# Kernel optimization log

Hardware: AMD Instinct MI355X
Metric: run time of the kernel (lower is better)

The kernel has to match this reference:

```python
import jax, jax.numpy as jnp
import numpy as np

B, N, F, U = 4, 4096, 256, 128
NEG = -1.0e9


def setup_inputs() -> dict:
    key = jax.random.key(0)
    k1, k2, k3, k4, k5 = jax.random.split(key, 5)
    inputs = jax.random.normal(k1, (B, N, F), dtype=jnp.float32)
    # Glorot-normal-like scales
    w = jax.random.normal(k2, (F, U), dtype=jnp.float32) * np.sqrt(2.0 / (F + U)).astype(np.float32)
    ai = jax.random.normal(k3, (U, N), dtype=jnp.float32) * np.sqrt(2.0 / (U + N)).astype(np.float32)
    aj = jax.random.normal(k4, (U, N), dtype=jnp.float32) * np.sqrt(2.0 / (U + N)).astype(np.float32)
    a = (jax.random.uniform(k5, (N, N)) < 0.004).astype(jnp.float32)
    adj = jnp.maximum(a, a.T)
    return {"inputs": inputs, "w": w, "ai": ai, "aj": aj, "adj": adj}


def reference(inputs, w, ai, aj, adj):
    # f: [B, N, U]
    f = jnp.einsum('bnf,fu->bnu', inputs, w)
    # self_attn[b,i,j] = (f ai)[b,i,j]; other_attn = transpose([0,2,1]) of (f aj)
    self_attn = jnp.einsum('bnu,um->bnm', f, ai)          # [B, N, N]
    other_attn = jnp.einsum('bnu,um->bmn', f, aj)         # transposed [B, N, N]
    mask = adj + jnp.eye(N, dtype=adj.dtype)              # allow self + neighbors
    attn = self_attn + other_attn + NEG * (1.0 - mask)
    attn = jax.nn.softmax(attn, axis=1)                   # softmax over rows (axis=1)
    # out[b,j,u] = sum_i f[b,i,u] * attn[b,i,j]
    out = jnp.einsum('biu,bij->bju', f, attn)
    return jax.nn.relu(out), attn
```

## Files before the change

kernel.cpp:

```cpp
#include <hip/hip_runtime.h>
#include <hip/hip_bf16.h>

#define NN 4096
#define UU 128
#define BB 4
#define FF 256
#define MAXD 128

__global__ __launch_bounds__(256) void transpose2(const float* __restrict__ ai,
                                                  const float* __restrict__ aj,
                                                  float* __restrict__ aiT,
                                                  float* __restrict__ ajT) {
    __shared__ float tile[32][33];
    const float* src = blockIdx.z ? aj : ai;
    float* dst = blockIdx.z ? ajT : aiT;
    int n0 = blockIdx.x * 32;
    int u0 = blockIdx.y * 32;
    int tx = threadIdx.x;
    int ty = threadIdx.y;
    for (int r = 0; r < 32; r += 8)
        tile[ty + r][tx] = src[(size_t)(u0 + ty + r) * NN + n0 + tx];
    __syncthreads();
    for (int r = 0; r < 32; r += 8)
        dst[(size_t)(n0 + ty + r) * UU + u0 + tx] = tile[tx][ty + r];
}

__global__ __launch_bounds__(256) void fgemm(const float* __restrict__ A,
                                             const float* __restrict__ Wm,
                                             float* __restrict__ F) {
    __shared__ float As[64][68];
    __shared__ float Ws[64][132];
    int t = threadIdx.x;
    int r0 = blockIdx.x * 64;
    int cg = t & 31;
    int rg = t >> 5;
    float acc[8][4] = {};

    for (int kc = 0; kc < FF; kc += 64) {
        {
            int row = t >> 2;
            int kb = (t & 3) * 16;
#pragma unroll
            for (int q = 0; q < 4; q++) {
                int kq = kb + q * 4;
                float4 v = *(const float4*)(A + (size_t)(r0 + row) * FF + kc + kq);
                As[kq + 0][row] = v.x; As[kq + 1][row] = v.y;
                As[kq + 2][row] = v.z; As[kq + 3][row] = v.w;
            }
        }
        {
#pragma unroll
            for (int q = 0; q < 8; q++) {
                int idx = q * 256 + t;
                int k = idx >> 5;
                int c4 = (idx & 31) * 4;
                *(float4*)&Ws[k][c4] = *(const float4*)(Wm + (size_t)(kc + k) * UU + c4);
            }
        }
        __syncthreads();
#pragma unroll 4
        for (int kk = 0; kk < 64; kk++) {
            float4 a0 = *(const float4*)&As[kk][rg * 8];
            float4 a1 = *(const float4*)&As[kk][rg * 8 + 4];
            float4 w4 = *(const float4*)&Ws[kk][cg * 4];
            float av[8] = {a0.x, a0.y, a0.z, a0.w, a1.x, a1.y, a1.z, a1.w};
#pragma unroll
            for (int i = 0; i < 8; i++) {
                acc[i][0] += av[i] * w4.x;
                acc[i][1] += av[i] * w4.y;
                acc[i][2] += av[i] * w4.z;
                acc[i][3] += av[i] * w4.w;
            }
        }
        __syncthreads();
    }
#pragma unroll
    for (int i = 0; i < 8; i++) {
        *(float4*)(F + (size_t)(r0 + rg * 8 + i) * UU + cg * 4) =
            make_float4(acc[i][0], acc[i][1], acc[i][2], acc[i][3]);
    }
}

__global__ __launch_bounds__(256) void scan_adj(const float* __restrict__ adj,
                                                unsigned short* __restrict__ csc,
                                                int* __restrict__ cnt,
                                                int* __restrict__ dblf) {
    __shared__ unsigned short tmp[MAXD];
    __shared__ int c, d;
    int j = blockIdx.x, tid = threadIdx.x;
    if (tid == 0) { c = 0; d = 0; }
    __syncthreads();
    const float4* row = (const float4*)(adj + (size_t)j * NN);
#pragma unroll
    for (int k = 0; k < 4; k++) {
        int q = tid + k * 256;
        float4 v = row[q];
        int base = q * 4;
        float vals[4] = {v.x, v.y, v.z, v.w};
#pragma unroll
        for (int t = 0; t < 4; t++) {
            int i = base + t;
            bool nz = (vals[t] != 0.0f);
            if (i == j) { if (nz) d = 1; nz = true; }
            if (nz) {
                int p = atomicAdd(&c, 1);
                if (p < MAXD) tmp[p] = (unsigned short)i;
            }
        }
    }
    __syncthreads();
    int M = c < MAXD ? c : MAXD;
    if (tid < M) csc[(size_t)j * MAXD + tid] = tmp[tid];
    if (tid == 0) { cnt[j] = M; dblf[j] = d; }
}

__global__ __launch_bounds__(256) void gat_cols(const unsigned short* __restrict__ csc,
                                                const int* __restrict__ cnt,
                                                const int* __restrict__ dblf,
                                                const float* __restrict__ f,
                                                const float* __restrict__ aiT,
                                                const float* __restrict__ ajT,
                                                float* __restrict__ out,
                                                float* __restrict__ attn) {
    __shared__ unsigned short sidx[MAXD];
    __shared__ float sex[BB][MAXD];
    int j = blockIdx.x, tid = threadIdx.x;
    int lane = tid & 63, b = tid >> 6;
    int M = cnt[j];
    int oneh = dblf[j];
    if (tid < M) sidx[tid] = csc[(size_t)j * MAXD + tid];

    const float* fb = f + (size_t)b * NN * UU;
    float2 fj = *(const float2*)(fb + (size_t)j * UU + 2 * lane);

    if (oneh) {
        if (lane == 0) attn[((size_t)(b * NN + j)) * NN + j] = 1.0f;
        float2 o;
        o.x = fj.x > 0.0f ? fj.x : 0.0f;
        o.y = fj.y > 0.0f ? fj.y : 0.0f;
        *(float2*)(out + ((size_t)(b * NN + j)) * UU + 2 * lane) = o;
        return;
    }
    __syncthreads();

    float2 ai2 = *(const float2*)(aiT + (size_t)j * UU + 2 * lane);
    float denom = 0.0f, acc0 = 0.0f, acc1 = 0.0f;
    for (int e = 0; e < M; e++) {
        int i = sidx[e];
        float2 fi  = *(const float2*)(fb + (size_t)i * UU + 2 * lane);
        float2 aj2 = *(const float2*)(ajT + (size_t)i * UU + 2 * lane);
        float p = fi.x * ai2.x + fi.y * ai2.y + fj.x * aj2.x + fj.y * aj2.y;
#pragma unroll
        for (int off = 32; off > 0; off >>= 1) p += __shfl_xor(p, off);
        float ex = __expf(p);
        denom += ex;
        acc0 += ex * fi.x;
        acc1 += ex * fi.y;
        if (lane == 0) sex[b][e] = ex;
    }
    float inv = 1.0f / denom;

    float2 o;
    o.x = acc0 * inv; o.y = acc1 * inv;
    o.x = o.x > 0.0f ? o.x : 0.0f;
    o.y = o.y > 0.0f ? o.y : 0.0f;
    *(float2*)(out + ((size_t)(b * NN + j)) * UU + 2 * lane) = o;

    __syncthreads();
    for (int e = lane; e < M; e += 64)
        attn[((size_t)(b * NN + sidx[e])) * NN + j] = sex[b][e] * inv;
}

extern "C" void kernel_launch(void* const* d_in, const int* in_sizes, int n_in,
                              void* d_out, int out_size, void* d_ws, size_t ws_size,
                              hipStream_t stream) {
    const float* inputs = (const float*)d_in[0];
    const float* w      = (const float*)d_in[1];
    const float* ai     = (const float*)d_in[2];
    const float* aj     = (const float*)d_in[3];
    const float* adj    = (const float*)d_in[4];

    float* out  = (float*)d_out;
    float* attn = out + (size_t)BB * NN * UU;

    float* f   = (float*)d_ws;
    float* aiT = f + (size_t)BB * NN * UU;
    float* ajT = aiT + (size_t)NN * UU;
    unsigned short* csc = (unsigned short*)(ajT + (size_t)NN * UU);
    int* cnt  = (int*)(csc + (size_t)NN * MAXD);
    int* dblf = cnt + NN;

    hipMemsetAsync(attn, 0, (size_t)BB * NN * NN * sizeof(float), stream);

    transpose2<<<dim3(NN / 32, UU / 32, 2), dim3(32, 8), 0, stream>>>(ai, aj, aiT, ajT);
    fgemm<<<dim3((BB * NN) / 64), 256, 0, stream>>>(inputs, w, f);
    scan_adj<<<NN, 256, 0, stream>>>(adj, csc, cnt, dblf);
    gat_cols<<<NN, 256, 0, stream>>>(csc, cnt, dblf, f, aiT, ajT, out, attn);
}
```

Before: 449.7 us.

## Batch neighbor loads and replace per-edge shuffle reductions with LDS chunked sums

The gat_cols edge loop is split into two passes. The first pass issues 16 neighbor feature loads per chunk, writes the partial dot products to LDS, and lets one lane per edge sum them and apply exp. The second pass accumulates the exp-weighted features in unrolled groups of 8. This removes the serial per-edge chain of load, wavefront shuffle reduction and exp, and exposes more memory-level parallelism. In exchange it reads the neighbor features twice (the second read likely hits cache), uses more LDS, and relies on wavefront-lockstep ordering of LDS writes and reads within each batch's wave, with no explicit barrier.

```diff
diff --git a/kernel.cpp b/kernel.cpp
--- a/kernel.cpp
+++ b/kernel.cpp
@@ -6,6 +6,7 @@
 #define BB 4
 #define FF 256
 #define MAXD 128
+#define CH 16
 
 __global__ __launch_bounds__(256) void transpose2(const float* __restrict__ ai,
                                                   const float* __restrict__ aj,
@@ -123,12 +124,13 @@
                                                 float* __restrict__ out,
                                                 float* __restrict__ attn) {
     __shared__ unsigned short sidx[MAXD];
-    __shared__ float sex[BB][MAXD];
+    __shared__ float sexp[BB][MAXD];
+    __shared__ float part[BB][CH][68];
     int j = blockIdx.x, tid = threadIdx.x;
     int lane = tid & 63, b = tid >> 6;
     int M = cnt[j];
     int oneh = dblf[j];
-    if (tid < M) sidx[tid] = csc[(size_t)j * MAXD + tid];
+    if (tid < MAXD) sidx[tid] = csc[(size_t)j * MAXD + tid];
 
     const float* fb = f + (size_t)b * NN * UU;
     float2 fj = *(const float2*)(fb + (size_t)j * UU + 2 * lane);
@@ -144,21 +146,45 @@
     __syncthreads();
 
     float2 ai2 = *(const float2*)(aiT + (size_t)j * UU + 2 * lane);
-    float denom = 0.0f, acc0 = 0.0f, acc1 = 0.0f;
-    for (int e = 0; e < M; e++) {
-        int i = sidx[e];
-        float2 fi  = *(const float2*)(fb + (size_t)i * UU + 2 * lane);
-        float2 aj2 = *(const float2*)(ajT + (size_t)i * UU + 2 * lane);
-        float p = fi.x * ai2.x + fi.y * ai2.y + fj.x * aj2.x + fj.y * aj2.y;
-#pragma unroll
-        for (int off = 32; off > 0; off >>= 1) p += __shfl_xor(p, off);
-        float ex = __expf(p);
-        denom += ex;
-        acc0 += ex * fi.x;
-        acc1 += ex * fi.y;
-        if (lane == 0) sex[b][e] = ex;
-    }
+    float denom = 0.0f;
+
+    for (int e0 = 0; e0 < M; e0 += CH) {
+#pragma unroll
+        for (int cc = 0; cc < CH; cc++) {
+            int ee = e0 + cc;
+            int i = sidx[ee < M ? ee : M - 1];
+            float2 fi  = *(const float2*)(fb + (size_t)i * UU + 2 * lane);
+            float2 aj2 = *(const float2*)(ajT + (size_t)i * UU + 2 * lane);
+            part[b][cc][lane] = fi.x * ai2.x + fi.y * ai2.y + fj.x * aj2.x + fj.y * aj2.y;
+        }
+        if (lane < CH && e0 + lane < M) {
+            float s = 0.0f;
+#pragma unroll
+            for (int q = 0; q < 16; q++) {
+                float4 v = *(const float4*)&part[b][lane][q * 4];
+                s += v.x + v.y + v.z + v.w;
+            }
+            float ex = __expf(s);
+            sexp[b][e0 + lane] = ex;
+            denom += ex;
+        }
+    }
+#pragma unroll
+    for (int off = 32; off > 0; off >>= 1) denom += __shfl_xor(denom, off);
     float inv = 1.0f / denom;
+
+    float acc0 = 0.0f, acc1 = 0.0f;
+    for (int e = 0; e < M; e += 8) {
+#pragma unroll
+        for (int q = 0; q < 8; q++) {
+            int ee = e + q;
+            float wgt = (ee < M) ? sexp[b][ee] : 0.0f;
+            int i = sidx[ee < M ? ee : 0];
+            float2 fi = *(const float2*)(fb + (size_t)i * UU + 2 * lane);
+            acc0 += wgt * fi.x;
+            acc1 += wgt * fi.y;
+        }
+    }
 
     float2 o;
     o.x = acc0 * inv; o.y = acc1 * inv;
@@ -166,9 +192,10 @@
     o.y = o.y > 0.0f ? o.y : 0.0f;
     *(float2*)(out + ((size_t)(b * NN + j)) * UU + 2 * lane) = o;
 
-    __syncthreads();
-    for (int e = lane; e < M; e += 64)
-        attn[((size_t)(b * NN + sidx[e])) * NN + j] = sex[b][e] * inv;
+    if (lane < M)
+        attn[((size_t)(b * NN + sidx[lane])) * NN + j] = sexp[b][lane] * inv;
+    if (lane + 64 < M)
+        attn[((size_t)(b * NN + sidx[lane + 64])) * NN + j] = sexp[b][lane + 64] * inv;
 }
 
 extern "C" void kernel_launch(void* const* d_in, const int* in_sizes, int n_in,
```

Result: slower. 460.2 us (+2.3%).
